# Kernel optimization log

Measured on AMD Instinct MI355X. Metric: run time of the kernel, lower is better.

Reference implementation:

```python
import jax, jax.numpy as jnp
import numpy as np

B, L, HID = 2, 2048, 2048
NH, NKV, HD = 16, 4, 128
LAT = 512
Q_PER_KV = NH // NKV
SCALE = HD ** -0.5
ROPE_THETA = 10000.0


def setup_inputs() -> dict:
    key = jax.random.key(0)
    ks = jax.random.split(key, 6)
    s = lambda fan_in: 1.0 / np.sqrt(fan_in)
    return {
        "x": jax.random.normal(ks[0], (B, L, HID), dtype=jnp.float32),
        "Wq": jax.random.normal(ks[1], (HID, NH * HD), dtype=jnp.float32) * s(HID),
        "Wc": jax.random.normal(ks[2], (HID, LAT), dtype=jnp.float32) * s(HID),
        "Wk": jax.random.normal(ks[3], (LAT, NKV * HD), dtype=jnp.float32) * s(LAT),
        "Wv": jax.random.normal(ks[4], (LAT, NKV * HD), dtype=jnp.float32) * s(LAT),
        "Wo": jax.random.normal(ks[5], (NH * HD, HID), dtype=jnp.float32) * s(NH * HD),
        "attention_mask": jnp.ones((B, L), dtype=jnp.int32),
    }


def _rope(t):  # t: [B, H, L, HD]
    half = HD // 2
    inv_freq = 1.0 / (ROPE_THETA ** (jnp.arange(half, dtype=jnp.float32) / half))
    pos = jnp.arange(t.shape[2], dtype=jnp.float32)
    freqs = pos[:, None] * inv_freq[None, :]          # [L, half]
    cos = jnp.cos(freqs)[None, None].astype(t.dtype)  # [1,1,L,half]
    sin = jnp.sin(freqs)[None, None].astype(t.dtype)
    t1, t2 = t[..., :half], t[..., half:]
    return jnp.concatenate([t1 * cos - t2 * sin, t2 * cos + t1 * sin], axis=-1)


def reference(x, Wq, Wc, Wk, Wv, Wo, attention_mask):
    q = (x @ Wq).reshape(B, L, NH, HD).transpose(0, 2, 1, 3)      # [B,NH,L,HD]
    c = x @ Wc                                                    # latent bottleneck
    k = (c @ Wk).reshape(B, L, NKV, HD).transpose(0, 2, 1, 3)     # [B,NKV,L,HD]
    v = (c @ Wv).reshape(B, L, NKV, HD).transpose(0, 2, 1, 3)
    # GQA repeat_interleave along head axis
    k = jnp.repeat(k, Q_PER_KV, axis=1)                           # [B,NH,L,HD]
    v = jnp.repeat(v, Q_PER_KV, axis=1)
    q = _rope(q)
    k = _rope(k)
    att = jnp.einsum("bhqd,bhkd->bhqk", q, k) * SCALE             # [B,NH,L,L]
    neg = jnp.finfo(att.dtype).min
    causal = jnp.tril(jnp.ones((L, L), dtype=bool))[None, None]
    att = jnp.where(causal, att, neg)
    key_mask = (attention_mask > 0)[:, None, None, :]             # [B,1,1,L]
    att = jnp.where(key_mask, att, neg)
    att = jax.nn.softmax(att, axis=-1)
    y = jnp.einsum("bhqk,bhkd->bhqd", att, v)
    y = y.transpose(0, 2, 1, 3).reshape(B, L, NH * HD)
    return y @ Wo
```

## Files before the change

kernel.cpp:

```cpp
#include <hip/hip_runtime.h>
#include <hip/hip_bf16.h>
#include <cstdint>
#include <cstddef>

#define B_    2
#define L_    2048
#define HID_  2048
#define NH_   16
#define NKV_  4
#define HD_   128
#define LAT_  512
#define SCALE_ 0.08838834764831845f
#define SC2_   0.1275174365f

typedef unsigned short u16;
typedef unsigned int   u32;
typedef __attribute__((ext_vector_type(8))) short   short8;
typedef __attribute__((ext_vector_type(4))) float   floatx4;

typedef __attribute__((address_space(1))) const u32 gas_u32;
typedef __attribute__((address_space(3))) u32       las_u32;

__device__ __forceinline__ void gl_lds16(const u16* g, u16* l) {
    __builtin_amdgcn_global_load_lds((gas_u32*)g, (las_u32*)l, 16, 0, 0);
}

__device__ __forceinline__ float bf2f(u16 u) {
    union { u32 i; float f; } v; v.i = ((u32)u) << 16; return v.f;
}
__device__ __forceinline__ u16 f2bf(float f) {
    union { float f; u32 u; } v; v.f = f;
    u32 u = v.u;
    u32 r = (u + 0x7fffu + ((u >> 16) & 1u)) >> 16;
    return (u16)r;
}

__global__ void cvt_kernel(const float* __restrict__ in, u16* __restrict__ out, int n) {
    int i = blockIdx.x * 256 + threadIdx.x;
    if (i < n) out[i] = f2bf(in[i]);
}

__global__ void cvt_transpose_kernel(const float* __restrict__ in, u16* __restrict__ out,
                                     int R, int C) {
    __shared__ u16 tile[32][33];
    int c0 = blockIdx.x * 32, r0 = blockIdx.y * 32;
    int tx = threadIdx.x & 31, ty = threadIdx.x >> 5;
    for (int i = ty; i < 32; i += 8)
        tile[tx][i] = f2bf(in[(size_t)(r0 + i) * C + c0 + tx]);
    __syncthreads();
    for (int i = ty; i < 32; i += 8)
        out[(size_t)(c0 + i) * R + r0 + tx] = tile[i][tx];
}

__global__ void transpose_v_kernel(const u16* __restrict__ in, u16* __restrict__ out) {
    __shared__ u16 t[32][33];
    int lt = blockIdx.x, dt = blockIdx.y, bh = blockIdx.z;
    int b = bh >> 2, kvh = bh & 3;
    int tx = threadIdx.x & 31, ty = threadIdx.x >> 5;
    for (int i = ty; i < 32; i += 8)
        t[i][tx] = in[(((size_t)b * L_ + lt * 32 + i) * NKV_ + kvh) * HD_ + dt * 32 + tx];
    __syncthreads();
    for (int i = ty; i < 32; i += 8)
        out[((size_t)bh * HD_ + dt * 32 + i) * L_ + lt * 32 + tx] = t[tx][i];
}

template<int OUT_BF16>
__global__ __launch_bounds__(256)
void gemm_bt(const u16* __restrict__ A, const u16* __restrict__ BT,
             void* __restrict__ C, int M, int N, int K) {
    __shared__ __align__(16) u16 As[128][32];
    __shared__ __align__(16) u16 Bs[128][32];
    const int tid  = threadIdx.x;
    const int m0   = blockIdx.y * 128, n0 = blockIdx.x * 128;
    const int wave = tid >> 6, lane = tid & 63;
    const int wm   = (wave >> 1) * 64, wn = (wave & 1) * 64;
    const int quad = lane >> 4, l16 = lane & 15;

    const int srow = wave * 32 + (lane >> 2);
    const int scol = (lane & 3) * 8;
    const u16* aptr0 = A  + (size_t)(m0 + srow) * K + scol;
    const u16* bptr0 = BT + (size_t)(n0 + srow) * K + scol;
    const u16* aptr1 = aptr0 + (size_t)16 * K;
    const u16* bptr1 = bptr0 + (size_t)16 * K;
    u16* lA0 = &As[wave * 32][0];
    u16* lA1 = &As[wave * 32 + 16][0];
    u16* lB0 = &Bs[wave * 32][0];
    u16* lB1 = &Bs[wave * 32 + 16][0];

    floatx4 acc[4][4] = {};

    for (int k0 = 0; k0 < K; k0 += 32) {
        gl_lds16(aptr0 + k0, lA0);
        gl_lds16(aptr1 + k0, lA1);
        gl_lds16(bptr0 + k0, lB0);
        gl_lds16(bptr1 + k0, lB1);
        __syncthreads();

        short8 af[4], bfr[4];
        #pragma unroll
        for (int i = 0; i < 4; i++) af[i]  = *(const short8*)&As[wm + i * 16 + l16][quad * 8];
        #pragma unroll
        for (int i = 0; i < 4; i++) bfr[i] = *(const short8*)&Bs[wn + i * 16 + l16][quad * 8];
        #pragma unroll
        for (int mi = 0; mi < 4; mi++)
            #pragma unroll
            for (int ni = 0; ni < 4; ni++)
                acc[mi][ni] = __builtin_amdgcn_mfma_f32_16x16x32_bf16(
                    af[mi], bfr[ni], acc[mi][ni], 0, 0, 0);
        __syncthreads();
    }

    #pragma unroll
    for (int mi = 0; mi < 4; mi++) {
        #pragma unroll
        for (int ni = 0; ni < 4; ni++) {
            #pragma unroll
            for (int r = 0; r < 4; r++) {
                int row = m0 + wm + mi * 16 + quad * 4 + r;
                int col = n0 + wn + ni * 16 + l16;
                float v = acc[mi][ni][r];
                if (OUT_BF16) ((u16*)C)[(size_t)row * N + col] = f2bf(v);
                else          ((float*)C)[(size_t)row * N + col] = v;
            }
        }
    }
}

__global__ __launch_bounds__(256)
void gemm_bt_split(const u16* __restrict__ A, const u16* __restrict__ BT,
                   u16* __restrict__ C0, u16* __restrict__ C1,
                   int M, int N, int K, int Nsplit, int N0, int N1) {
    __shared__ __align__(16) u16 As[128][32];
    __shared__ __align__(16) u16 Bs[128][32];
    const int tid  = threadIdx.x;
    const int m0   = blockIdx.y * 128, n0 = blockIdx.x * 128;
    const int wave = tid >> 6, lane = tid & 63;
    const int wm   = (wave >> 1) * 64, wn = (wave & 1) * 64;
    const int quad = lane >> 4, l16 = lane & 15;

    const int srow = wave * 32 + (lane >> 2);
    const int scol = (lane & 3) * 8;
    const u16* aptr0 = A  + (size_t)(m0 + srow) * K + scol;
    const u16* bptr0 = BT + (size_t)(n0 + srow) * K + scol;
    const u16* aptr1 = aptr0 + (size_t)16 * K;
    const u16* bptr1 = bptr0 + (size_t)16 * K;
    u16* lA0 = &As[wave * 32][0];
    u16* lA1 = &As[wave * 32 + 16][0];
    u16* lB0 = &Bs[wave * 32][0];
    u16* lB1 = &Bs[wave * 32 + 16][0];

    floatx4 acc[4][4] = {};

    for (int k0 = 0; k0 < K; k0 += 32) {
        gl_lds16(aptr0 + k0, lA0);
        gl_lds16(aptr1 + k0, lA1);
        gl_lds16(bptr0 + k0, lB0);
        gl_lds16(bptr1 + k0, lB1);
        __syncthreads();

        short8 af[4], bfr[4];
        #pragma unroll
        for (int i = 0; i < 4; i++) af[i]  = *(const short8*)&As[wm + i * 16 + l16][quad * 8];
        #pragma unroll
        for (int i = 0; i < 4; i++) bfr[i] = *(const short8*)&Bs[wn + i * 16 + l16][quad * 8];
        #pragma unroll
        for (int mi = 0; mi < 4; mi++)
            #pragma unroll
            for (int ni = 0; ni < 4; ni++)
                acc[mi][ni] = __builtin_amdgcn_mfma_f32_16x16x32_bf16(
                    af[mi], bfr[ni], acc[mi][ni], 0, 0, 0);
        __syncthreads();
    }

    const int side = (n0 >= Nsplit);
    u16* Cw = side ? C1 : C0;
    const int nw = side ? N1 : N0;
    const int cbase = side ? Nsplit : 0;

    #pragma unroll
    for (int mi = 0; mi < 4; mi++) {
        #pragma unroll
        for (int ni = 0; ni < 4; ni++) {
            #pragma unroll
            for (int r = 0; r < 4; r++) {
                int row = m0 + wm + mi * 16 + quad * 4 + r;
                int col = n0 + wn + ni * 16 + l16 - cbase;
                Cw[(size_t)row * nw + col] = f2bf(acc[mi][ni][r]);
            }
        }
    }
}

__global__ void rope_perm(const u16* __restrict__ in, u16* __restrict__ out,
                          int nh, int nhbits) {
    int idx = blockIdx.x * 256 + threadIdx.x;
    int d = idx & 63;
    int l = (idx >> 6) & (L_ - 1);
    int h = (idx >> 17) & (nh - 1);
    int b = idx >> (17 + nhbits);
    const u16* src = &in[(((size_t)b * L_ + l) * nh + h) * HD_];
    u16* dst = &out[(((size_t)b * nh + h) * L_ + l) * HD_];
    float t1 = bf2f(src[d]), t2 = bf2f(src[d + 64]);
    float inv = expf(-(float)d * 0.14391156831212787f);
    float fr = (float)l * inv;
    float c = cosf(fr), sn = sinf(fr);
    dst[d]      = f2bf(t1 * c - t2 * sn);
    dst[d + 64] = f2bf(t2 * c + t1 * sn);
}

__global__ __launch_bounds__(256)
void attn_mfma(const u16* __restrict__ Q, const u16* __restrict__ K,
               const u16* __restrict__ Vt, const int* __restrict__ amask,
               u16* __restrict__ Y, float* __restrict__ Opart,
               float* __restrict__ lpart) {
    __shared__ __align__(16) u16 Ks[64][128];
    __shared__ __align__(16) u16 Vs[128][64];
    __shared__ int smask[64];

    const int tid  = threadIdx.x;
    const int wave = tid >> 6, lane = tid & 63;
    const int quad = lane >> 4, l16 = lane & 15;

    const int bid = blockIdx.x;
    const int s   = bid >> 8;
    const int c   = bid & 255;
    const int bkvh = c & 7;
    const int j   = c >> 3;
    const int b   = bkvh >> 2, kvh = bkvh & 3;

    const int H  = ((32 + j) >> 1) + 1;
    const int Lg = ((31 - j) >> 1) + 1;
    const int m2 = max((H + 1) >> 1, (Lg + 1) >> 1);
    const int m3 = max((H + 2) / 3, Lg);
    const int nh = (m2 <= m3) ? 2 : 3;
    const int nl = 4 - nh;
    int t, kt0, kt1, pi;
    if (s < nh) {
        t = 32 + j; kt0 = (H * s) / nh; kt1 = (H * (s + 1)) / nh; pi = bid;
    } else {
        t = 31 - j;
        const int ls = s - nh;
        kt0 = (Lg * ls) / nl; kt1 = (Lg * (ls + 1)) / nl;
        pi = (nl == 1) ? -1 : bid;
    }

    const int h   = kvh * 4 + wave;
    const int q0  = t * 32;

    const u16* Qbase = Q  + ((size_t)b * NH_  + h)   * L_ * HD_;
    const u16* Kbase = K  + ((size_t)b * NKV_ + kvh) * L_ * HD_;
    const u16* Vbase = Vt + ((size_t)b * NKV_ + kvh) * (size_t)HD_ * L_;
    const int* mbase = amask + b * L_;

    short8 qa[2][4];
    #pragma unroll
    for (int mi = 0; mi < 2; ++mi)
        #pragma unroll
        for (int ks = 0; ks < 4; ++ks)
            qa[mi][ks] = *(const short8*)&Qbase[(size_t)(q0 + mi * 16 + l16) * HD_ + ks * 32 + quad * 8];

    floatx4 Oacc[2][8] = {};
    float lsum[2][4] = {};

    const int krow = tid >> 2, kq0 = (tid & 3) * 4;
    const int vrow = tid >> 1, vc0 = (tid & 1) * 4;
    const int kr7  = krow & 7, vr7 = vrow & 7;
    u16* kdst0 = &Ks[krow][((kq0 + 0) ^ kr7) * 8];
    u16* kdst1 = &Ks[krow][((kq0 + 1) ^ kr7) * 8];
    u16* kdst2 = &Ks[krow][((kq0 + 2) ^ kr7) * 8];
    u16* kdst3 = &Ks[krow][((kq0 + 3) ^ kr7) * 8];
    u16* vdst0 = &Vs[vrow][((vc0 + 0) ^ vr7) * 8];
    u16* vdst1 = &Vs[vrow][((vc0 + 1) ^ vr7) * 8];
    u16* vdst2 = &Vs[vrow][((vc0 + 2) ^ vr7) * 8];
    u16* vdst3 = &Vs[vrow][((vc0 + 3) ^ vr7) * 8];
    const u16* ksrc = Kbase + ((size_t)(kt0 * 64 + krow)) * HD_ + kq0 * 8;
    const u16* vsrc = Vbase + (size_t)vrow * L_ + kt0 * 64 + vc0 * 8;

    u16* Psb = &Ks[0][0] + wave * 2048;

    const int fr_rd = ((l16 >> 2) & 3) ^ ((l16 & 3) << 1);

    for (int kt = kt0; kt < kt1; ++kt) {
        const int kbase = kt * 64;

        *(uint4*)kdst0 = *(const uint4*)(ksrc);
        *(uint4*)kdst1 = *(const uint4*)(ksrc + 8);
        *(uint4*)kdst2 = *(const uint4*)(ksrc + 16);
        *(uint4*)kdst3 = *(const uint4*)(ksrc + 24);
        *(uint4*)vdst0 = *(const uint4*)(vsrc);
        *(uint4*)vdst1 = *(const uint4*)(vsrc + 8);
        *(uint4*)vdst2 = *(const uint4*)(vsrc + 16);
        *(uint4*)vdst3 = *(const uint4*)(vsrc + 24);
        if (tid < 64) smask[tid] = mbase[kbase + tid];
        ksrc += (size_t)64 * HD_;
        vsrc += 64;
        __syncthreads();

        floatx4 sfr[2][4] = {};
        __builtin_amdgcn_s_setprio(1);
        #pragma unroll
        for (int ni = 0; ni < 4; ++ni) {
            #pragma unroll
            for (int ks = 0; ks < 4; ++ks) {
                short8 kf = *(const short8*)&Ks[ni * 16 + l16][((ks * 4 + quad) ^ (l16 & 7)) * 8];
                sfr[0][ni] = __builtin_amdgcn_mfma_f32_16x16x32_bf16(qa[0][ks], kf, sfr[0][ni], 0, 0, 0);
                sfr[1][ni] = __builtin_amdgcn_mfma_f32_16x16x32_bf16(qa[1][ks], kf, sfr[1][ni], 0, 0, 0);
            }
        }
        __builtin_amdgcn_s_setprio(0);

        int am[4];
        #pragma unroll
        for (int ni = 0; ni < 4; ++ni) am[ni] = smask[ni * 16 + l16];

        __syncthreads();

        #pragma unroll
        for (int mi = 0; mi < 2; ++mi) {
            #pragma unroll
            for (int ni = 0; ni < 4; ++ni) {
                const int kpos = kbase + ni * 16 + l16;
                const bool okm = am[ni] > 0;
                const int blk_log = ni * 2 + (l16 >> 3);
                const int off = l16 & 7;
                #pragma unroll
                for (int r = 0; r < 4; ++r) {
                    const int qrow = q0 + mi * 16 + quad * 4 + r;
                    const bool ok = (kpos <= qrow) & okm;
                    float p = ok ? exp2f(fmaf(sfr[mi][ni][r], SC2_, -8.0f)) : 0.0f;
                    lsum[mi][r] += p;
                    const int pblk = blk_log ^ quad ^ (r << 1);
                    Psb[(mi * 16 + quad * 4 + r) * 64 + pblk * 8 + off] = f2bf(p);
                }
            }
        }

        short8 pf[2][2];
        #pragma unroll
        for (int mi = 0; mi < 2; ++mi)
            #pragma unroll
            for (int kc = 0; kc < 2; ++kc)
                pf[mi][kc] = *(const short8*)&Psb[(mi * 16 + l16) * 64 + ((kc * 4 + quad) ^ fr_rd) * 8];

        __builtin_amdgcn_s_setprio(1);
        #pragma unroll
        for (int kc = 0; kc < 2; ++kc) {
            #pragma unroll
            for (int dn = 0; dn < 8; ++dn) {
                short8 vf = *(const short8*)&Vs[dn * 16 + l16][((kc * 4 + quad) ^ (l16 & 7)) * 8];
                Oacc[0][dn] = __builtin_amdgcn_mfma_f32_16x16x32_bf16(pf[0][kc], vf, Oacc[0][dn], 0, 0, 0);
                Oacc[1][dn] = __builtin_amdgcn_mfma_f32_16x16x32_bf16(pf[1][kc], vf, Oacc[1][dn], 0, 0, 0);
            }
        }
        __builtin_amdgcn_s_setprio(0);
        __syncthreads();
    }

    if (pi < 0) {
        #pragma unroll
        for (int mi = 0; mi < 2; ++mi) {
            #pragma unroll
            for (int r = 0; r < 4; ++r) {
                float v = lsum[mi][r];
                v += __shfl_xor(v, 1);
                v += __shfl_xor(v, 2);
                v += __shfl_xor(v, 4);
                v += __shfl_xor(v, 8);
                const float linv = 1.0f / v;
                const int qrow = q0 + mi * 16 + quad * 4 + r;
                u16* dst = &Y[(((size_t)b * L_ + qrow) * NH_ + h) * HD_];
                #pragma unroll
                for (int dn = 0; dn < 8; ++dn)
                    dst[dn * 16 + l16] = f2bf(Oacc[mi][dn][r] * linv);
            }
        }
    } else {
        float* od = Opart + ((size_t)pi * 4 + wave) * 32 * 128;
        float* lp = lpart + ((size_t)pi * 4 + wave) * 32;
        #pragma unroll
        for (int mi = 0; mi < 2; ++mi) {
            #pragma unroll
            for (int r = 0; r < 4; ++r) {
                float v = lsum[mi][r];
                v += __shfl_xor(v, 1);
                v += __shfl_xor(v, 2);
                v += __shfl_xor(v, 4);
                v += __shfl_xor(v, 8);
                const int qi = mi * 16 + quad * 4 + r;
                if (l16 == 0) __builtin_nontemporal_store(v, &lp[qi]);
                #pragma unroll
                for (int dn = 0; dn < 8; ++dn)
                    __builtin_nontemporal_store(Oacc[mi][dn][r],
                                                &od[(size_t)qi * 128 + dn * 16 + l16]);
            }
        }
    }
}

__global__ __launch_bounds__(256)
void attn_combine(const float* __restrict__ Opart, const float* __restrict__ lpart,
                  u16* __restrict__ Y) {
    const int cb = blockIdx.x;
    const int c  = cb & 255, z = cb >> 8;
    const int tile = z >> 2, hw = z & 3;
    const int bkvh = c & 7, j = c >> 3;
    const int b = bkvh >> 2, kvh = bkvh & 3;
    const int h = kvh * 4 + hw;
    const int H  = ((32 + j) >> 1) + 1;
    const int Lg = ((31 - j) >> 1) + 1;
    const int m2 = max((H + 1) >> 1, (Lg + 1) >> 1);
    const int m3 = max((H + 2) / 3, Lg);
    const int nh = (m2 <= m3) ? 2 : 3;
    const int nl = 4 - nh;
    if (tile == 1 && nl == 1) return;
    const int s0 = tile ? nh : 0;
    const int ns = tile ? nl : nh;
    const int t  = tile ? (31 - j) : (32 + j);
    const int tid = threadIdx.x;
    const int q = tid >> 3, dg = tid & 7;

    float4 a0 = {0,0,0,0}, a1 = {0,0,0,0}, a2 = {0,0,0,0}, a3 = {0,0,0,0};
    float lacc = 0.0f;
    for (int i = 0; i < ns; ++i) {
        const size_t rowb = ((size_t)((s0 + i) * 256 + c) * 4 + hw) * 32 + q;
        lacc += lpart[rowb];
        const float4* op = (const float4*)(Opart + rowb * 128 + dg * 16);
        float4 v0 = op[0], v1 = op[1], v2 = op[2], v3 = op[3];
        a0.x += v0.x; a0.y += v0.y; a0.z += v0.z; a0.w += v0.w;
        a1.x += v1.x; a1.y += v1.y; a1.z += v1.z; a1.w += v1.w;
        a2.x += v2.x; a2.y += v2.y; a2.z += v2.z; a2.w += v2.w;
        a3.x += v3.x; a3.y += v3.y; a3.z += v3.z; a3.w += v3.w;
    }
    const float linv = 1.0f / lacc;
    const int qrow = t * 32 + q;
    u16* dst = &Y[(((size_t)b * L_ + qrow) * NH_ + h) * HD_ + dg * 16];

    u16 tmp[16];
    tmp[0]  = f2bf(a0.x * linv); tmp[1]  = f2bf(a0.y * linv);
    tmp[2]  = f2bf(a0.z * linv); tmp[3]  = f2bf(a0.w * linv);
    tmp[4]  = f2bf(a1.x * linv); tmp[5]  = f2bf(a1.y * linv);
    tmp[6]  = f2bf(a1.z * linv); tmp[7]  = f2bf(a1.w * linv);
    tmp[8]  = f2bf(a2.x * linv); tmp[9]  = f2bf(a2.y * linv);
    tmp[10] = f2bf(a2.z * linv); tmp[11] = f2bf(a2.w * linv);
    tmp[12] = f2bf(a3.x * linv); tmp[13] = f2bf(a3.y * linv);
    tmp[14] = f2bf(a3.z * linv); tmp[15] = f2bf(a3.w * linv);
    *(uint4*)(dst)     = *(const uint4*)(&tmp[0]);
    *(uint4*)(dst + 8) = *(const uint4*)(&tmp[8]);
}

extern "C" void kernel_launch(void* const* d_in, const int* in_sizes, int n_in,
                              void* d_out, int out_size, void* d_ws, size_t ws_size,
                              hipStream_t stream) {
    const float* x  = (const float*)d_in[0];
    const float* Wq = (const float*)d_in[1];
    const float* Wc = (const float*)d_in[2];
    const float* Wk = (const float*)d_in[3];
    const float* Wv = (const float*)d_in[4];
    const float* Wo = (const float*)d_in[5];
    const int* amask = (const int*)d_in[6];
    float* out = (float*)d_out;

    char* p = (char*)d_ws;
    auto alloc = [&](size_t elems) {
        u16* r = (u16*)p;
        p += ((elems * 2 + 255) / 256) * 256;
        return r;
    };
    u16* WoT  = alloc((size_t)2048 * 2048);
    u16* qbuf = alloc((size_t)4096 * 2048);
    u16* Qr   = alloc((size_t)4096 * 2048);
    u16* Kr   = alloc((size_t)4096 * 512);
    u16* Vt   = alloc((size_t)4096 * 512);
    char* pdead = p;
    u16* Xb   = alloc((size_t)4096 * 2048);
    u16* WqT  = alloc((size_t)2048 * 2048);
    u16* WcT  = alloc((size_t)512 * 2048);
    u16* WkT  = alloc((size_t)512 * 512);
    u16* WvT  = alloc((size_t)512 * 512);
    u16* cbuf = alloc((size_t)4096 * 512);
    u16* kbuf = alloc((size_t)4096 * 512);
    u16* vbuf = alloc((size_t)4096 * 512);
    float* Opart = (float*)pdead;
    float* lpart = (float*)(pdead + (size_t)1024 * 4 * 32 * 128 * 4);

    cvt_kernel<<<8388608 / 256, 256, 0, stream>>>(x, Xb, 8388608);
    cvt_transpose_kernel<<<dim3(2048 / 32, 2048 / 32), 256, 0, stream>>>(Wq, WqT, 2048, 2048);
    cvt_transpose_kernel<<<dim3(512 / 32, 2048 / 32), 256, 0, stream>>>(Wc, WcT, 2048, 512);
    cvt_transpose_kernel<<<dim3(512 / 32, 512 / 32), 256, 0, stream>>>(Wk, WkT, 512, 512);
    cvt_transpose_kernel<<<dim3(512 / 32, 512 / 32), 256, 0, stream>>>(Wv, WvT, 512, 512);
    cvt_transpose_kernel<<<dim3(2048 / 32, 2048 / 32), 256, 0, stream>>>(Wo, WoT, 2048, 2048);

    gemm_bt_split<<<dim3(20, 32), 256, 0, stream>>>(Xb, WqT, qbuf, cbuf,
                                                    4096, 2560, 2048, 2048, 2048, 512);
    gemm_bt_split<<<dim3(8, 32), 256, 0, stream>>>(cbuf, WkT, kbuf, vbuf,
                                                   4096, 1024, 512, 512, 512, 512);

    rope_perm<<<(2 * 16 * 2048 * 64) / 256, 256, 0, stream>>>(qbuf, Qr, 16, 4);
    rope_perm<<<(2 * 4 * 2048 * 64) / 256, 256, 0, stream>>>(kbuf, Kr, 4, 2);
    transpose_v_kernel<<<dim3(64, 4, 8), 256, 0, stream>>>(vbuf, Vt);

    attn_mfma<<<dim3(1024), 256, 0, stream>>>(Qr, Kr, Vt, amask, qbuf, Opart, lpart);
    attn_combine<<<dim3(2048), 256, 0, stream>>>(Opart, lpart, qbuf);

    gemm_bt<0><<<dim3(16, 32), 256, 0, stream>>>(qbuf, WoT, out, 4096, 2048, 2048);
}
```

Measured before the change: 388.9 us.

## Permute V columns to pack P stores as 8-byte writes; vectorize x conversion

The V transpose now writes its key columns in a permuted order. This lets each lane pack its four P values for one row into a single 8-byte LDS store with a new XOR swizzle, replacing sixteen scalar stores, and the fragment reads are adjusted to match. P conversion switches to the hardware bf16 intrinsic, and the fp32-to-bf16 conversion of x now uses float4 loads and 8-byte stores. The aim is to cut LDS store instructions in the attention inner loop and raise bandwidth efficiency in the conversion kernel, at the cost of a coupled layout contract between the V transpose and the attention kernel that must stay consistent.

```diff
diff --git a/kernel.cpp b/kernel.cpp
--- a/kernel.cpp
+++ b/kernel.cpp
@@ -34,10 +34,21 @@
     u32 r = (u + 0x7fffu + ((u >> 16) & 1u)) >> 16;
     return (u16)r;
 }
-
-__global__ void cvt_kernel(const float* __restrict__ in, u16* __restrict__ out, int n) {
+__device__ __forceinline__ u16 f2bf_hw(float f) {
+    union { __hip_bfloat16 h; u16 u; } c;
+    c.h = __float2bfloat16(f);
+    return c.u;
+}
+
+__global__ void cvt_kernel(const float* __restrict__ in, u16* __restrict__ out, int n4) {
     int i = blockIdx.x * 256 + threadIdx.x;
-    if (i < n) out[i] = f2bf(in[i]);
+    if (i < n4) {
+        float4 v = ((const float4*)in)[i];
+        union { u16 w[4]; uint2 v; } o;
+        o.w[0] = f2bf(v.x); o.w[1] = f2bf(v.y);
+        o.w[2] = f2bf(v.z); o.w[3] = f2bf(v.w);
+        ((uint2*)out)[i] = o.v;
+    }
 }
 
 __global__ void cvt_transpose_kernel(const float* __restrict__ in, u16* __restrict__ out,
@@ -60,8 +71,10 @@
     for (int i = ty; i < 32; i += 8)
         t[i][tx] = in[(((size_t)b * L_ + lt * 32 + i) * NKV_ + kvh) * HD_ + dt * 32 + tx];
     __syncthreads();
+    const int lcol = lt * 32 + tx;
+    const int csig = (lcol & ~63) | ((lcol & 15) << 2) | ((lcol >> 4) & 3);
     for (int i = ty; i < 32; i += 8)
-        out[((size_t)bh * HD_ + dt * 32 + i) * L_ + lt * 32 + tx] = t[tx][i];
+        out[((size_t)bh * HD_ + dt * 32 + i) * L_ + csig] = t[tx][i];
 }
 
 template<int OUT_BF16>
@@ -278,8 +291,6 @@
 
     u16* Psb = &Ks[0][0] + wave * 2048;
 
-    const int fr_rd = ((l16 >> 2) & 3) ^ ((l16 & 3) << 1);
-
     for (int kt = kt0; kt < kt1; ++kt) {
         const int kbase = kt * 64;
 
@@ -318,20 +329,19 @@
         #pragma unroll
         for (int mi = 0; mi < 2; ++mi) {
             #pragma unroll
-            for (int ni = 0; ni < 4; ++ni) {
-                const int kpos = kbase + ni * 16 + l16;
-                const bool okm = am[ni] > 0;
-                const int blk_log = ni * 2 + (l16 >> 3);
-                const int off = l16 & 7;
+            for (int r = 0; r < 4; ++r) {
+                const int qrow = q0 + mi * 16 + quad * 4 + r;
+                union { u16 w[4]; uint2 v; } pb;
                 #pragma unroll
-                for (int r = 0; r < 4; ++r) {
-                    const int qrow = q0 + mi * 16 + quad * 4 + r;
-                    const bool ok = (kpos <= qrow) & okm;
+                for (int ni = 0; ni < 4; ++ni) {
+                    const int kpos = kbase + ni * 16 + l16;
+                    const bool ok = (kpos <= qrow) & (am[ni] > 0);
                     float p = ok ? exp2f(fmaf(sfr[mi][ni][r], SC2_, -8.0f)) : 0.0f;
                     lsum[mi][r] += p;
-                    const int pblk = blk_log ^ quad ^ (r << 1);
-                    Psb[(mi * 16 + quad * 4 + r) * 64 + pblk * 8 + off] = f2bf(p);
+                    pb.w[ni] = f2bf_hw(p);
                 }
+                const int row = mi * 16 + quad * 4 + r;
+                *(uint2*)&Psb[row * 64 + ((l16 ^ ((row & 7) << 1)) << 2)] = pb.v;
             }
         }
 
@@ -339,8 +349,11 @@
         #pragma unroll
         for (int mi = 0; mi < 2; ++mi)
             #pragma unroll
-            for (int kc = 0; kc < 2; ++kc)
-                pf[mi][kc] = *(const short8*)&Psb[(mi * 16 + l16) * 64 + ((kc * 4 + quad) ^ fr_rd) * 8];
+            for (int kc = 0; kc < 2; ++kc) {
+                const int row = mi * 16 + l16;
+                const int p0 = (kc * 8 + quad * 2) ^ ((l16 & 7) << 1);
+                pf[mi][kc] = *(const short8*)&Psb[row * 64 + p0 * 4];
+            }
 
         __builtin_amdgcn_s_setprio(1);
         #pragma unroll
@@ -483,7 +496,7 @@
     float* Opart = (float*)pdead;
     float* lpart = (float*)(pdead + (size_t)1024 * 4 * 32 * 128 * 4);
 
-    cvt_kernel<<<8388608 / 256, 256, 0, stream>>>(x, Xb, 8388608);
+    cvt_kernel<<<8388608 / 4 / 256, 256, 0, stream>>>(x, Xb, 8388608 / 4);
     cvt_transpose_kernel<<<dim3(2048 / 32, 2048 / 32), 256, 0, stream>>>(Wq, WqT, 2048, 2048);
     cvt_transpose_kernel<<<dim3(512 / 32, 2048 / 32), 256, 0, stream>>>(Wc, WcT, 2048, 512);
     cvt_transpose_kernel<<<dim3(512 / 32, 512 / 32), 256, 0, stream>>>(Wk, WkT, 512, 512);
```

Result: faster. 374.2 us (-3.8%).
